# Performance work log

Hardware: AMD Instinct MI355X
Metric: run time of the kernel (lower is better)

## Reference

```python
import jax, jax.numpy as jnp
import numpy as np

B, C, N, K, L = 4, 256, 8192, 4, 3


def _mlp2(h, W1, b1, W2, b2):
    return jax.nn.relu(h @ W1 + b1) @ W2 + b2


def setup_inputs() -> dict:
    key = jax.random.key(0)
    ks = jax.random.split(key, 12)
    s = lambda fan_in: 1.0 / np.sqrt(fan_in)
    inp = {
        "x": jax.random.normal(ks[0], (B, C, N), jnp.float32),
        "points": jax.random.normal(ks[1], (N, 3), jnp.float32),
        "neighbors": jax.random.randint(ks[2], (N, K), 0, N, jnp.int32),
        "edge_W1": jax.random.normal(ks[3], (3, C // 4), jnp.float32) * s(3),
        "edge_b1": jnp.zeros((C // 4,), jnp.float32),
        "edge_W2": jax.random.normal(ks[4], (C // 4, C // 2), jnp.float32) * s(C // 4),
        "edge_b2": jnp.zeros((C // 2,), jnp.float32),
        "msg_W1": jax.random.normal(ks[5], (L, 2 * C + C // 2, 2 * C), jnp.float32) * s(2 * C + C // 2),
        "msg_b1": jnp.zeros((L, 2 * C), jnp.float32),
        "msg_W2": jax.random.normal(ks[6], (L, 2 * C, C), jnp.float32) * s(2 * C),
        "msg_b2": jnp.zeros((L, C), jnp.float32),
        "upd_W1": jax.random.normal(ks[7], (L, 2 * C, 2 * C), jnp.float32) * s(2 * C),
        "upd_b1": jnp.zeros((L, 2 * C), jnp.float32),
        "upd_W2": jax.random.normal(ks[8], (L, 2 * C, C), jnp.float32) * s(2 * C),
        "upd_b2": jnp.zeros((L, C), jnp.float32),
    }
    return inp


def reference(x, points, neighbors, edge_W1, edge_b1, edge_W2, edge_b2,
              msg_W1, msg_b1, msg_W2, msg_b2, upd_W1, upd_b1, upd_W2, upd_b2):
    # x: [B, C, N] -> features [B, N, C]
    feats = jnp.transpose(x, (0, 2, 1))
    # edge features shared across layers: [N, K, C//2]
    edge_vec = points[neighbors] - points[:, None, :]          # [N, K, 3]
    edge_feat = _mlp2(edge_vec, edge_W1, edge_b1, edge_W2, edge_b2)
    for l in range(L):
        sender = feats[:, neighbors, :]                         # [B, N, K, C]
        receiver = jnp.broadcast_to(feats[:, :, None, :], sender.shape)
        ef = jnp.broadcast_to(edge_feat[None], (feats.shape[0],) + edge_feat.shape)
        msg_in = jnp.concatenate([sender, receiver, ef], axis=-1)  # [B,N,K,2.5C]
        msg = _mlp2(msg_in, msg_W1[l], msg_b1[l], msg_W2[l], msg_b2[l])
        agg = jnp.mean(msg, axis=2)                             # [B, N, C]
        upd_in = jnp.concatenate([feats, agg], axis=-1)         # [B, N, 2C]
        feats = _mlp2(upd_in, upd_W1[l], upd_b1[l], upd_W2[l], upd_b2[l])
    return jnp.transpose(feats, (0, 2, 1))
```

## Files before the change

### kernel.cpp

```cpp
#include <hip/hip_runtime.h>

#define DEVI __device__ __forceinline__

typedef unsigned short u16;
typedef unsigned int   u32;
typedef __attribute__((ext_vector_type(8))) short short8;
typedef __attribute__((ext_vector_type(4))) short short4b;
typedef __attribute__((ext_vector_type(4))) float f32x4;

DEVI float bf2f(u16 u) {
    union { u32 i; float f; } x; x.i = ((u32)u) << 16; return x.f;
}
DEVI u16 f2bf(float f) {
    u32 u = __float_as_uint(f);
    u32 r = (u + 0x7FFFu + ((u >> 16) & 1u)) >> 16;
    return (u16)r;
}

DEVI void gload_lds16(const void* g, void* l) {
    __builtin_amdgcn_global_load_lds((const __attribute__((address_space(1))) void*)g,
                                     (__attribute__((address_space(3))) void*)l, 16, 0, 0);
}

struct PJob { u32 dst, soff, tbase, ld, Kd, src; };
__device__ const PJob g_jobs[19] = {
    {0,        0,      0,    128, 64,  4},
    {8192,     0,      8,    512, 256, 0},
    {139264,   131072, 136,  512, 256, 0},
    {270336,   262144, 264,  512, 128, 0},
    {335872,   0,      328,  256, 512, 1},
    {466944,   0,      456,  512, 512, 2},
    {729088,   0,      712,  256, 512, 3},
    {860160,   327680, 840,  512, 256, 0},
    {991232,   458752, 968,  512, 256, 0},
    {1122304,  589824, 1096, 512, 128, 0},
    {1187840,  131072, 1160, 256, 512, 1},
    {1318912,  262144, 1288, 512, 512, 2},
    {1581056,  131072, 1544, 256, 512, 3},
    {1712128,  655360, 1672, 512, 256, 0},
    {1843200,  786432, 1800, 512, 256, 0},
    {1974272,  917504, 1928, 512, 128, 0},
    {2039808,  262144, 1992, 256, 512, 1},
    {2170880,  524288, 2120, 512, 512, 2},
    {2433024,  262144, 2376, 256, 512, 3},
};

__global__ __launch_bounds__(256) void setup_kernel(
    const float* __restrict__ x, u16* __restrict__ feats,
    const float* __restrict__ points, const int* __restrict__ nb,
    const float* __restrict__ eW1, const float* __restrict__ eb1,
    u16* __restrict__ hEdge,
    const float* __restrict__ mW1, const float* __restrict__ mW2,
    const float* __restrict__ uW1, const float* __restrict__ uW2,
    const float* __restrict__ eW2,
    u16* __restrict__ wreg, u16* __restrict__ mW2bf)
{
    __shared__ float tile[32][33];
    int bid = blockIdx.x;
    int t = threadIdx.x;
    int tx = t & 31, ty = t >> 5;

    if (bid < 2504) {
        int ji = 0;
        #pragma unroll
        for (int i = 1; i < 19; ++i) if (bid >= (int)g_jobs[i].tbase) ji = i;
        PJob jb = g_jobs[ji];
        const float* src = (jb.src == 0) ? mW1 : (jb.src == 1) ? mW2 : (jb.src == 2) ? uW1
                         : (jb.src == 3) ? uW2 : eW2;
        src += jb.soff;
        int tt = bid - (int)jb.tbase;
        int nk = (int)jb.Kd >> 5;
        int tk = tt % nk, tj = tt / nk;
        int k0 = tk * 32, j0 = tj * 32;
        #pragma unroll
        for (int yy = 0; yy < 4; ++yy) {
            int k = k0 + ty + yy * 8;
            tile[ty + yy * 8][tx] = src[(size_t)k * jb.ld + j0 + tx];
        }
        __syncthreads();
        u16* dst = wreg + jb.dst;
        #pragma unroll
        for (int yy = 0; yy < 4; ++yy) {
            int j = j0 + ty + yy * 8;
            dst[(size_t)j * jb.Kd + k0 + tx] = f2bf(tile[tx][ty + yy * 8]);
        }
    } else if (bid < 10696) {
        int bb = bid - 2504;
        int n0 = (bb & 255) * 32, c0 = ((bb >> 8) & 7) * 32, b = bb >> 11;
        #pragma unroll
        for (int yy = 0; yy < 4; ++yy) {
            int c = c0 + ty + yy * 8;
            tile[ty + yy * 8][tx] = x[((size_t)b * 256 + c) * 8192 + n0 + tx];
        }
        __syncthreads();
        #pragma unroll
        for (int yy = 0; yy < 4; ++yy) {
            int n = n0 + ty + yy * 8;
            feats[((size_t)b * 8192 + n) * 256 + c0 + tx] = f2bf(tile[tx][ty + yy * 8]);
        }
    } else if (bid < 10824) {
        int e = (bid - 10696) * 256 + t;
        int n = e >> 2;
        int j2 = nb[e];
        float p0x = points[n * 3], p0y = points[n * 3 + 1], p0z = points[n * 3 + 2];
        float v0 = points[j2 * 3]     - p0x;
        float v1 = points[j2 * 3 + 1] - p0y;
        float v2 = points[j2 * 3 + 2] - p0z;
        #pragma unroll
        for (int jb2 = 0; jb2 < 8; ++jb2) {
            short8 o;
            #pragma unroll
            for (int jj = 0; jj < 8; ++jj) {
                int j = jb2 * 8 + jj;
                float hv = v0 * eW1[j] + v1 * eW1[64 + j] + v2 * eW1[128 + j] + eb1[j];
                o[jj] = (short)f2bf(fmaxf(hv, 0.0f));
            }
            *(short8*)&hEdge[(size_t)e * 64 + jb2 * 8] = o;
        }
    } else {
        int i = (bid - 10824) * 256 + t;
        float4 v = *(const float4*)&mW2[(size_t)i * 4];
        short4b o;
        o[0] = (short)f2bf(v.x); o[1] = (short)f2bf(v.y);
        o[2] = (short)f2bf(v.z); o[3] = (short)f2bf(v.w);
        *(short4b*)&mW2bf[(size_t)i * 4] = o;
    }
}

__global__ __launch_bounds__(256) void biasfix(const u16* __restrict__ wreg,
    const float* __restrict__ mb2, const float* __restrict__ ub1,
    float* __restrict__ ub1c)
{
    int idx = blockIdx.x * 256 + threadIdx.x;
    int l = idx >> 9, n = idx & 511;
    const u16* U1T = wreg + 8192 + l * 851968 + 458752;
    const float* b2 = mb2 + l * 256;
    float s = ub1[l * 512 + n];
    for (int j0 = 0; j0 < 256; j0 += 8) {
        short8 wv = *(const short8*)&U1T[(size_t)n * 512 + 256 + j0];
        #pragma unroll
        for (int jj = 0; jj < 8; ++jj) s += bf2f((u16)wv[jj]) * b2[j0 + jj];
    }
    ub1c[idx] = s;
}

struct GArgs {
    const u16* A1; const u16* A2; const u16* B1; const u16* B2;
    const float* bias; u16* C;
    long sA, sB, sC;
    int lda1, K1, lda2, ldb1, ldb2, ldc, nbn, Ktot, relu, permrows, transout, bpb;
};

__global__ __launch_bounds__(512, 4) void gemm_bt(GArgs g0, GArgs g1, int nbx0)
{
    __shared__ u16 lds[32768];
    int bx0 = (int)blockIdx.x;
    bool j0 = bx0 < nbx0;
    GArgs g = j0 ? g0 : g1;
    int nwgj = j0 ? nbx0 : ((int)gridDim.x - nbx0);
    int bxl  = j0 ? bx0 : bx0 - nbx0;

    const u16* A1 = g.A1; const u16* A2 = g.A2;
    const u16* B1 = g.B1; const u16* B2 = g.B2;
    u16* Cp = g.C;
    if (g.bpb > 0) {
        int by = bxl / g.bpb;
        bxl -= by * g.bpb;
        nwgj = g.bpb;
        A1 += (long)by * g.sA; A2 += (long)by * g.sA;
        B1 += (long)by * g.sB; B2 += (long)by * g.sB;
        Cp += (long)by * g.sC;
    }
    int bx = (bxl & 7) * (nwgj >> 3) + (bxl >> 3);
    int tn = bx % g.nbn, tm = bx / g.nbn;
    int t = threadIdx.x;
    int l = t & 63, w = t >> 6;
    int wrow = (w >> 2) * 64, wcol = (w & 3) * 32;
    int lm = l & 15, lk = l >> 4;
    int swz = lm & 7;
    int rowA = tm * 128;
    int rowB = tn * 128;

    f32x4 acc[4][2];
    #pragma unroll
    for (int mi = 0; mi < 4; ++mi)
        #pragma unroll
        for (int ni = 0; ni < 2; ++ni)
            acc[mi][ni] = (f32x4){0.f, 0.f, 0.f, 0.f};

    int nks  = g.Ktot >> 6;
    int nksw = (g.K1 < g.Ktot) ? (g.K1 >> 6) : 0x7fffffff;

    int rr[2], cc[2];
    const u16* pA[2]; const u16* pB[2];
    #pragma unroll
    for (int i = 0; i < 2; ++i) {
        int chunk = i * 512 + t;
        rr[i] = chunk >> 3;
        cc[i] = (chunk & 7) ^ (rr[i] & 7);
        pA[i] = A1 + (size_t)(rowA + rr[i]) * g.lda1 + cc[i] * 8;
        pB[i] = B1 + (size_t)(rowB + rr[i]) * g.ldb1 + cc[i] * 8;
    }
    int st = 0;
    auto STAGE = [&]() {
        if (st == nksw) {
            #pragma unroll
            for (int i = 0; i < 2; ++i) {
                pA[i] = A2 + (size_t)(rowA + rr[i]) * g.lda2 + cc[i] * 8;
                pB[i] = B2 + (size_t)(rowB + rr[i]) * g.ldb2 + cc[i] * 8;
            }
        }
        u16* At = lds + (st & 1) * 16384;
        u16* Bt = At + 8192;
        #pragma unroll
        for (int i = 0; i < 2; ++i) {
            int chunk = i * 512 + t;
            gload_lds16(pA[i], &At[chunk * 8]); pA[i] += 64;
            gload_lds16(pB[i], &Bt[chunk * 8]); pB[i] += 64;
        }
        ++st;
    };

    STAGE();
    if (nks > 1) STAGE();
    int cur = 0;
    for (int ks = 0; ks < nks; ++ks) {
        if (ks + 1 < nks) asm volatile("s_waitcnt vmcnt(4)\n\ts_barrier" ::: "memory");
        else              asm volatile("s_waitcnt vmcnt(0)\n\ts_barrier" ::: "memory");
        const u16* At = lds + cur * 16384;
        const u16* Bt = At + 8192;
        __builtin_amdgcn_s_setprio(1);
        #pragma unroll
        for (int ksub = 0; ksub < 2; ++ksub) {
            int sOff = (((ksub << 2) | lk) ^ swz) << 3;
            short8 af[4], bv[2];
            #pragma unroll
            for (int mi = 0; mi < 4; ++mi)
                af[mi] = *(const short8*)&At[(wrow + mi * 16 + lm) * 64 + sOff];
            #pragma unroll
            for (int ni = 0; ni < 2; ++ni)
                bv[ni] = *(const short8*)&Bt[(wcol + ni * 16 + lm) * 64 + sOff];
            #pragma unroll
            for (int mi = 0; mi < 4; ++mi)
                #pragma unroll
                for (int ni = 0; ni < 2; ++ni)
                    acc[mi][ni] = __builtin_amdgcn_mfma_f32_16x16x32_bf16(af[mi], bv[ni], acc[mi][ni], 0, 0, 0);
        }
        __builtin_amdgcn_s_setprio(0);
        asm volatile("s_barrier" ::: "memory");
        if (st < nks) STAGE();
        cur ^= 1;
    }

    int str = g.transout ? 134 : 136;
    #pragma unroll
    for (int ni = 0; ni < 2; ++ni) {
        int col = wcol + ni * 16 + lm;
        float bvl = g.bias ? g.bias[tn * 128 + col] : 0.0f;
        #pragma unroll
        for (int mi = 0; mi < 4; ++mi) {
            int row0 = wrow + mi * 16 + lk * 4;
            f32x4 v = acc[mi][ni];
            #pragma unroll
            for (int r = 0; r < 4; ++r) {
                float f = v[r] + bvl;
                if (g.relu) f = fmaxf(f, 0.0f);
                lds[(row0 + r) * str + col] = f2bf(f);
            }
        }
    }
    __syncthreads();
    if (g.transout) {
        float* Co = (float*)Cp;
        int b  = tm >> 6;
        int n0 = (tm & 63) * 128;
        int c0 = tn * 128;
        #pragma unroll
        for (int p = 0; p < 32; ++p) {
            int row = (t & 63) + ((p & 1) << 6);
            int col = (t >> 6) + ((p >> 1) << 3);
            float f = bf2f(lds[row * 134 + col]);
            Co[((size_t)b * 256 + c0 + col) * 8192 + n0 + row] = f;
        }
    } else {
        #pragma unroll
        for (int p = 0; p < 4; ++p) {
            int chunk = p * 512 + t;
            int row = chunk >> 4, sl = chunk & 15;
            short8 v = *(const short8*)&lds[row * 136 + sl * 8];
            int m = tm * 128 + row;
            int orow = g.permrows ? (((m & 8191) << 2) | (m >> 13)) : m;
            *(short8*)&Cp[(size_t)orow * g.ldc + tn * 128 + sl * 8] = v;
        }
    }
}

__global__ __launch_bounds__(256, 3) void gather_relu_mean(
    const u16* __restrict__ PR, const u16* __restrict__ E,
    const int* __restrict__ nb, const float* __restrict__ b1,
    u16* __restrict__ hbar)
{
    int b = threadIdx.x >> 6, l = threadIdx.x & 63;
    int c0 = l * 8;
    int n0 = blockIdx.x * 4;

    int nbarr[4][4];
    #pragma unroll
    for (int ii = 0; ii < 4; ++ii) {
        int4 v = *(const int4*)&nb[(n0 + ii) * 4];
        nbarr[ii][0] = v.x; nbarr[ii][1] = v.y; nbarr[ii][2] = v.z; nbarr[ii][3] = v.w;
    }

    short8 pv[4][4];
    #pragma unroll
    for (int ii = 0; ii < 4; ++ii)
        #pragma unroll
        for (int k = 0; k < 4; ++k)
            pv[ii][k] = *(const short8*)&PR[(size_t)(nbarr[ii][k] * 4 + b) * 1024 + c0];
    short8 rv[4];
    #pragma unroll
    for (int ii = 0; ii < 4; ++ii)
        rv[ii] = *(const short8*)&PR[(size_t)((n0 + ii) * 4 + b) * 1024 + 512 + c0];

    float4 b1a = *(const float4*)&b1[c0];
    float4 b1b = *(const float4*)&b1[c0 + 4];
    float bb[8] = {b1a.x, b1a.y, b1a.z, b1a.w, b1b.x, b1b.y, b1b.z, b1b.w};

    #pragma unroll
    for (int ii = 0; ii < 4; ++ii) {
        int n = n0 + ii;
        short8 ev[4];
        #pragma unroll
        for (int k = 0; k < 4; ++k)
            ev[k] = *(const short8*)&E[(size_t)(n * 4 + k) * 512 + c0];

        float base[8], acc[8];
        #pragma unroll
        for (int j = 0; j < 8; ++j) { base[j] = bf2f((u16)rv[ii][j]) + bb[j]; acc[j] = 0.0f; }
        #pragma unroll
        for (int k = 0; k < 4; ++k) {
            #pragma unroll
            for (int j = 0; j < 8; ++j) {
                float v = bf2f((u16)pv[ii][k][j]) + bf2f((u16)ev[k][j]) + base[j];
                acc[j] += fmaxf(v, 0.0f);
            }
        }
        short8 o;
        #pragma unroll
        for (int j = 0; j < 8; ++j) o[j] = (short)f2bf(acc[j] * 0.25f);
        *(short8*)&hbar[((size_t)(b << 13) + n) * 512 + c0] = o;
    }
}

static inline GArgs mkargs(const u16* A1, int lda1, int K1, const u16* A2, int lda2,
                           const u16* B1, int ldb1, const u16* B2, int ldb2,
                           const float* bias, u16* C, int ldc,
                           int nbn, int Ktot, int relu, int permrows,
                           int transout = 0, int bpb = 0,
                           long sA = 0, long sB = 0, long sC = 0)
{
    GArgs g;
    g.A1 = A1; g.A2 = A2; g.B1 = B1; g.B2 = B2; g.bias = bias; g.C = C;
    g.sA = sA; g.sB = sB; g.sC = sC;
    g.lda1 = lda1; g.K1 = K1; g.lda2 = lda2; g.ldb1 = ldb1; g.ldb2 = ldb2;
    g.ldc = ldc; g.nbn = nbn; g.Ktot = Ktot; g.relu = relu; g.permrows = permrows;
    g.transout = transout; g.bpb = bpb;
    return g;
}

extern "C" void kernel_launch(void* const* d_in, const int* in_sizes, int n_in,
                              void* d_out, int out_size, void* d_ws, size_t ws_size,
                              hipStream_t stream)
{
    const float* x      = (const float*)d_in[0];
    const float* points = (const float*)d_in[1];
    const int*   nb     = (const int*)d_in[2];
    const float* eW1    = (const float*)d_in[3];
    const float* eb1    = (const float*)d_in[4];
    const float* eW2    = (const float*)d_in[5];
    const float* eb2    = (const float*)d_in[6];
    const float* mW1    = (const float*)d_in[7];
    const float* mb1    = (const float*)d_in[8];
    const float* mW2    = (const float*)d_in[9];
    const float* mb2    = (const float*)d_in[10];
    const float* uW1    = (const float*)d_in[11];
    const float* ub1    = (const float*)d_in[12];
    const float* uW2    = (const float*)d_in[13];
    const float* ub2    = (const float*)d_in[14];
    float* out = (float*)d_out;

    char* ws = (char*)d_ws;
    u16* featsA = (u16*)(ws);
    u16* featsB = (u16*)(ws + 16777216);
    u16* ef     = (u16*)(ws + 33554432);
    u16* PR     = (u16*)(ws + 41943040);
    u16* E      = (u16*)(ws + 109051904);
    u16* hbar   = (u16*)(ws + 142606336);
    u16* wreg   = (u16*)(ws + 176160768);
    u16*   mW2bf = (u16*)(ws + 181288960);
    u16*   WcT   = (u16*)(ws + 182075392);
    float* ub1c  = (float*)(ws + 183648256);
    u16* hEdge  = PR;
    u16* H2     = PR;
    u16* agg    = E;

    const bool fused = (ws_size >= 183654400ull);

    setup_kernel<<<fused ? 11208 : 10824, 256, 0, stream>>>(
        x, featsA, points, nb, eW1, eb1, hEdge,
        mW1, mW2, uW1, uW2, eW2, wreg, mW2bf);

    if (fused) {
        biasfix<<<6, 256, 0, stream>>>(wreg, mb2, ub1, ub1c);
        const u16* U1T0 = wreg + 8192 + 458752;
        GArgs gef = mkargs(hEdge, 64, 64, hEdge, 64, wreg, 64, wreg, 64,
                           eb2, ef, 128, 1, 64, 0, 0);
        GArgs gwc = mkargs(U1T0 + 256, 512, 256, U1T0, 512, mW2bf, 256, mW2bf, 256,
                           nullptr, WcT, 512, 4, 256, 0, 0, 0, 16,
                           851968, 131072, 262144);
        gemm_bt<<<304, 512, 0, stream>>>(gef, gwc, 256);
    } else {
        GArgs gef = mkargs(hEdge, 64, 64, hEdge, 64, wreg, 64, wreg, 64,
                           eb2, ef, 128, 1, 64, 0, 0);
        gemm_bt<<<256, 512, 0, stream>>>(gef, gef, 256);
    }

    const u16* fin = featsA; u16* fout = featsB;
    for (int lyr = 0; lyr < 3; ++lyr) {
        u16* W1abT = wreg + 8192 + lyr * 851968;
        u16* W1cT  = W1abT + 262144;
        u16* W2T   = W1abT + 327680;
        u16* U1T   = W1abT + 458752;
        u16* U2T   = W1abT + 720896;
        const float* b1  = mb1 + lyr * 512;
        const float* b2  = mb2 + lyr * 256;
        const float* u1b = ub1 + lyr * 512;
        const float* u2b = ub2 + lyr * 256;
        const bool last = (lyr == 2);

        {
            GArgs gPR = mkargs((const u16*)fin, 256, 256, (const u16*)fin, 256,
                               W1abT, 256, W1abT, 256, nullptr, PR, 1024, 8, 256, 0, 1);
            GArgs gE  = mkargs(ef, 128, 128, ef, 128, W1cT, 128, W1cT, 128,
                               nullptr, E, 512, 4, 128, 0, 0);
            gemm_bt<<<3072, 512, 0, stream>>>(gPR, gE, 2048);
        }
        gather_relu_mean<<<2048, 256, 0, stream>>>(PR, E, nb, b1, hbar);

        if (fused) {
            GArgs g = mkargs((const u16*)fin, 256, 256, hbar, 512,
                             U1T, 512, WcT + lyr * 262144, 512,
                             ub1c + lyr * 512, H2, 512, 4, 768, 1, 0);
            gemm_bt<<<1024, 512, 0, stream>>>(g, g, 1024);
        } else {
            GArgs ga = mkargs(hbar, 512, 512, hbar, 512, W2T, 512, W2T, 512,
                              b2, agg, 256, 2, 512, 0, 0);
            gemm_bt<<<512, 512, 0, stream>>>(ga, ga, 512);
            GArgs gh = mkargs((const u16*)fin, 256, 256, agg, 256,
                              U1T, 512, U1T + 256, 512,
                              u1b, H2, 512, 4, 512, 1, 0);
            gemm_bt<<<1024, 512, 0, stream>>>(gh, gh, 1024);
        }
        {
            GArgs g = mkargs(H2, 512, 512, H2, 512, U2T, 512, U2T, 512,
                             u2b, last ? (u16*)out : fout, 256, 2, 512, 0, 0,
                             last ? 1 : 0);
            gemm_bt<<<512, 512, 0, stream>>>(g, g, 512);
        }

        const u16* tmp = fin; fin = fout; fout = (u16*)tmp;
    }
}
```

Before: 400.9 us.

## Add persistent BK=32 GEMM that prefetches next tile during epilogue for PR/E

Adds a persistent GEMM kernel, gemm_bt_p, in which each of 1024 workgroups processes three 128x128 output tiles. It uses BK=32 double-buffered LDS (32 KB instead of 64 KB) so more workgroups fit per CU (launch bounds 512,6), and it issues the first global-to-LDS loads of the next tile while the current tile's epilogue stores are in flight. It replaces the 3072-block gemm_bt launch for the per-layer PR/E projection. The cost is more barrier iterations per K and a single ksub per stage. The epilogue now reuses the same LDS as the staging buffers. The gemm_bt changes are cosmetic constant renames.

```diff
diff --git a/kernel.cpp b/kernel.cpp
--- a/kernel.cpp
+++ b/kernel.cpp
@@ -153,6 +153,8 @@
 
 __global__ __launch_bounds__(512, 4) void gemm_bt(GArgs g0, GArgs g1, int nbx0)
 {
+    constexpr int BK = 64;
+    constexpr int BUFU = 256 * BK;
     __shared__ u16 lds[32768];
     int bx0 = (int)blockIdx.x;
     bool j0 = bx0 < nbx0;
@@ -177,7 +179,6 @@
     int l = t & 63, w = t >> 6;
     int wrow = (w >> 2) * 64, wcol = (w & 3) * 32;
     int lm = l & 15, lk = l >> 4;
-    int swz = lm & 7;
     int rowA = tm * 128;
     int rowB = tn * 128;
 
@@ -188,18 +189,19 @@
         for (int ni = 0; ni < 2; ++ni)
             acc[mi][ni] = (f32x4){0.f, 0.f, 0.f, 0.f};
 
-    int nks  = g.Ktot >> 6;
-    int nksw = (g.K1 < g.Ktot) ? (g.K1 >> 6) : 0x7fffffff;
+    int nks  = g.Ktot / BK;
+    int nksw = (g.K1 < g.Ktot) ? (g.K1 / BK) : 0x7fffffff;
 
     int rr[2], cc[2];
     const u16* pA[2]; const u16* pB[2];
     #pragma unroll
     for (int i = 0; i < 2; ++i) {
         int chunk = i * 512 + t;
-        rr[i] = chunk >> 3;
-        cc[i] = (chunk & 7) ^ (rr[i] & 7);
-        pA[i] = A1 + (size_t)(rowA + rr[i]) * g.lda1 + cc[i] * 8;
-        pB[i] = B1 + (size_t)(rowB + rr[i]) * g.ldb1 + cc[i] * 8;
+        int r = chunk >> 3, s = chunk & 7;
+        int c = s ^ (r & 7);
+        rr[i] = r; cc[i] = c;
+        pA[i] = A1 + (size_t)(rowA + r) * g.lda1 + c * 8;
+        pB[i] = B1 + (size_t)(rowB + r) * g.ldb1 + c * 8;
     }
     int st = 0;
     auto STAGE = [&]() {
@@ -210,13 +212,13 @@
                 pB[i] = B2 + (size_t)(rowB + rr[i]) * g.ldb2 + cc[i] * 8;
             }
         }
-        u16* At = lds + (st & 1) * 16384;
-        u16* Bt = At + 8192;
+        u16* At = lds + (st & 1) * BUFU;
+        u16* Bt = At + 128 * BK;
         #pragma unroll
         for (int i = 0; i < 2; ++i) {
             int chunk = i * 512 + t;
-            gload_lds16(pA[i], &At[chunk * 8]); pA[i] += 64;
-            gload_lds16(pB[i], &Bt[chunk * 8]); pB[i] += 64;
+            gload_lds16(pA[i], &At[chunk * 8]); pA[i] += BK;
+            gload_lds16(pB[i], &Bt[chunk * 8]); pB[i] += BK;
         }
         ++st;
     };
@@ -227,19 +229,19 @@
     for (int ks = 0; ks < nks; ++ks) {
         if (ks + 1 < nks) asm volatile("s_waitcnt vmcnt(4)\n\ts_barrier" ::: "memory");
         else              asm volatile("s_waitcnt vmcnt(0)\n\ts_barrier" ::: "memory");
-        const u16* At = lds + cur * 16384;
-        const u16* Bt = At + 8192;
+        const u16* At = lds + cur * BUFU;
+        const u16* Bt = At + 128 * BK;
         __builtin_amdgcn_s_setprio(1);
         #pragma unroll
         for (int ksub = 0; ksub < 2; ++ksub) {
-            int sOff = (((ksub << 2) | lk) ^ swz) << 3;
+            int sOff = (((ksub << 2) | lk) ^ (lm & 7)) << 3;
             short8 af[4], bv[2];
             #pragma unroll
             for (int mi = 0; mi < 4; ++mi)
-                af[mi] = *(const short8*)&At[(wrow + mi * 16 + lm) * 64 + sOff];
+                af[mi] = *(const short8*)&At[(wrow + mi * 16 + lm) * BK + sOff];
             #pragma unroll
             for (int ni = 0; ni < 2; ++ni)
-                bv[ni] = *(const short8*)&Bt[(wcol + ni * 16 + lm) * 64 + sOff];
+                bv[ni] = *(const short8*)&Bt[(wcol + ni * 16 + lm) * BK + sOff];
             #pragma unroll
             for (int mi = 0; mi < 4; ++mi)
                 #pragma unroll
@@ -291,6 +293,133 @@
             int m = tm * 128 + row;
             int orow = g.permrows ? (((m & 8191) << 2) | (m >> 13)) : m;
             *(short8*)&Cp[(size_t)orow * g.ldc + tn * 128 + sl * 8] = v;
+        }
+    }
+}
+
+__global__ __launch_bounds__(512, 6) void gemm_bt_p(GArgs g0, GArgs g1, int nbx0, int R)
+{
+    __shared__ u16 lds[16384];
+    int G = (int)gridDim.x;
+    int t = threadIdx.x;
+    int l = t & 63, w = t >> 6;
+    int wrow = (w >> 2) * 64, wcol = (w & 3) * 32;
+    int lm = l & 15, lk = l >> 4;
+    int sOff = (lk ^ ((lm >> 1) & 3)) << 3;
+    int rS = t >> 2;
+    int cS = (t & 3) ^ ((rS >> 1) & 3);
+
+    for (int r = 0; r < R; ++r) {
+        int tid = (int)blockIdx.x + r * G;
+        bool j0 = tid < nbx0;
+        GArgs g = j0 ? g0 : g1;
+        int nwgj = j0 ? nbx0 : (G * R - nbx0);
+        int bxl  = j0 ? tid : tid - nbx0;
+        int bx = (bxl & 7) * (nwgj >> 3) + (bxl >> 3);
+        int tn = bx % g.nbn, tm = bx / g.nbn;
+        int rowA = tm * 128, rowB = tn * 128;
+        const u16* pA = g.A1 + (size_t)(rowA + rS) * g.lda1 + cS * 8;
+        const u16* pB = g.B1 + (size_t)(rowB + rS) * g.ldb1 + cS * 8;
+        int nks = g.Ktot >> 5;
+
+        if (r == 0) {
+            gload_lds16(pA, &lds[t * 8]);        pA += 32;
+            gload_lds16(pB, &lds[4096 + t * 8]); pB += 32;
+            gload_lds16(pA, &lds[8192 + t * 8]);  pA += 32;
+            gload_lds16(pB, &lds[12288 + t * 8]); pB += 32;
+        } else {
+            pA += 64; pB += 64;
+        }
+        int st = 2;
+
+        f32x4 acc[4][2];
+        #pragma unroll
+        for (int mi = 0; mi < 4; ++mi)
+            #pragma unroll
+            for (int ni = 0; ni < 2; ++ni)
+                acc[mi][ni] = (f32x4){0.f, 0.f, 0.f, 0.f};
+
+        int cur = 0;
+        for (int ks = 0; ks < nks; ++ks) {
+            if (ks + 1 < nks) asm volatile("s_waitcnt vmcnt(2)\n\ts_barrier" ::: "memory");
+            else              asm volatile("s_waitcnt vmcnt(0)\n\ts_barrier" ::: "memory");
+            const u16* At = lds + cur * 8192;
+            const u16* Bt = At + 4096;
+            __builtin_amdgcn_s_setprio(1);
+            {
+                short8 af[4], bv[2];
+                #pragma unroll
+                for (int mi = 0; mi < 4; ++mi)
+                    af[mi] = *(const short8*)&At[(wrow + mi * 16 + lm) * 32 + sOff];
+                #pragma unroll
+                for (int ni = 0; ni < 2; ++ni)
+                    bv[ni] = *(const short8*)&Bt[(wcol + ni * 16 + lm) * 32 + sOff];
+                #pragma unroll
+                for (int mi = 0; mi < 4; ++mi)
+                    #pragma unroll
+                    for (int ni = 0; ni < 2; ++ni)
+                        acc[mi][ni] = __builtin_amdgcn_mfma_f32_16x16x32_bf16(af[mi], bv[ni], acc[mi][ni], 0, 0, 0);
+            }
+            __builtin_amdgcn_s_setprio(0);
+            asm volatile("s_barrier" ::: "memory");
+            if (st < nks) {
+                u16* At2 = lds + (st & 1) * 8192;
+                gload_lds16(pA, &At2[t * 8]);        pA += 32;
+                gload_lds16(pB, &At2[4096 + t * 8]); pB += 32;
+                ++st;
+            }
+            cur ^= 1;
+        }
+
+        #pragma unroll
+        for (int ni = 0; ni < 2; ++ni) {
+            int col = wcol + ni * 16 + lm;
+            float bvl = g.bias ? g.bias[tn * 128 + col] : 0.0f;
+            #pragma unroll
+            for (int mi = 0; mi < 4; ++mi) {
+                int row0 = wrow + mi * 16 + lk * 4;
+                f32x4 v = acc[mi][ni];
+                #pragma unroll
+                for (int rw = 0; rw < 4; ++rw) {
+                    float f = v[rw] + bvl;
+                    if (g.relu) f = fmaxf(f, 0.0f);
+                    lds[(row0 + rw) * 128 + col] = f2bf(f);
+                }
+            }
+        }
+        asm volatile("s_waitcnt lgkmcnt(0)\n\ts_barrier" ::: "memory");
+        short8 ev[4];
+        int rowp[4];
+        #pragma unroll
+        for (int p = 0; p < 4; ++p) {
+            int chunk = p * 512 + t;
+            int row = chunk >> 4, sl = chunk & 15;
+            rowp[p] = row;
+            ev[p] = *(const short8*)&lds[row * 128 + sl * 8];
+        }
+        asm volatile("s_waitcnt lgkmcnt(0)\n\ts_barrier" ::: "memory");
+        #pragma unroll
+        for (int p = 0; p < 4; ++p) {
+            int chunk = p * 512 + t;
+            int sl = chunk & 15;
+            int m = tm * 128 + rowp[p];
+            int orow = g.permrows ? (((m & 8191) << 2) | (m >> 13)) : m;
+            *(short8*)&g.C[(size_t)orow * g.ldc + tn * 128 + sl * 8] = ev[p];
+        }
+        if (r + 1 < R) {
+            int tid2 = tid + G;
+            bool j02 = tid2 < nbx0;
+            GArgs g2 = j02 ? g0 : g1;
+            int nwgj2 = j02 ? nbx0 : (G * R - nbx0);
+            int bxl2  = j02 ? tid2 : tid2 - nbx0;
+            int bx2 = (bxl2 & 7) * (nwgj2 >> 3) + (bxl2 >> 3);
+            int tn2 = bx2 % g2.nbn, tm2 = bx2 / g2.nbn;
+            const u16* qA = g2.A1 + (size_t)(tm2 * 128 + rS) * g2.lda1 + cS * 8;
+            const u16* qB = g2.B1 + (size_t)(tn2 * 128 + rS) * g2.ldb1 + cS * 8;
+            gload_lds16(qA, &lds[t * 8]);
+            gload_lds16(qB, &lds[4096 + t * 8]);
+            gload_lds16(qA + 32, &lds[8192 + t * 8]);
+            gload_lds16(qB + 32, &lds[12288 + t * 8]);
         }
     }
 }
@@ -443,7 +572,7 @@
                                W1abT, 256, W1abT, 256, nullptr, PR, 1024, 8, 256, 0, 1);
             GArgs gE  = mkargs(ef, 128, 128, ef, 128, W1cT, 128, W1cT, 128,
                                nullptr, E, 512, 4, 128, 0, 0);
-            gemm_bt<<<3072, 512, 0, stream>>>(gPR, gE, 2048);
+            gemm_bt_p<<<1024, 512, 0, stream>>>(gPR, gE, 2048, 3);
         }
         gather_relu_mean<<<2048, 256, 0, stream>>>(PR, E, nb, b1, hbar);
 
```

New measurement: 402.2 us. About the same (+0.3%).
